# Kernel tuning notes

Measured on AMD Instinct MI355X. Metric: run time of the kernel, lower is better.

Reference implementation:

```python
import jax, jax.numpy as jnp
import numpy as np

T_STEPS = 4000          # T_ms / dt = 1000 / 0.25
N_IN, N_OUT = 64, 10
HID = [1024, 1024]
DT, TAU = 0.25, 10.0
BETA = float(np.exp(-DT / TAU))   # beta_snn
THR = 1.0                          # thr_snn
SLOPE = 1.0                        # spike_snn uses slope=1.0
W_STD = 32.0                       # W_STD_CUBA

@jax.custom_vjp
def spike(u):
    # SurrogateSpike.forward: heaviside on (mem - thr)
    return (u >= 0).astype(u.dtype)

def _spike_fwd(u):
    return spike(u), u

def _spike_bwd(u, g):
    # fast-sigmoid surrogate: slope / (1 + slope*|u|)^2
    grad = SLOPE / (1.0 + SLOPE * jnp.abs(u)) ** 2
    return (g * grad,)

spike.defvjp(_spike_fwd, _spike_bwd)

def setup_inputs() -> dict:
    key = jax.random.key(0)
    ks = jax.random.split(key, 8)
    B = 16
    # Bernoulli(0.05) input spike train, time-major [T, B, N_IN]
    input_spikes = (jax.random.uniform(ks[0], (T_STEPS, B, N_IN)) < 0.05).astype(jnp.float32)
    sizes = [N_IN] + HID + [N_OUT]
    inp = {"input_spikes": input_spikes}
    for i, (n_pre, n_post) in enumerate(zip(sizes[:-1], sizes[1:])):
        # init_weight 'normal': clamp(N(0, W_STD), min=0) / n_pre
        w = jnp.maximum(jax.random.normal(ks[i + 1], (n_pre, n_post)) * W_STD, 0.0) / n_pre
        inp[f"W{i}"] = w.astype(jnp.float32)
        inp[f"b{i}"] = jnp.zeros((n_post,), jnp.float32)
    return inp

def reference(input_spikes, W0, b0, W1, b1, W2, b2):
    # Dale's law: feedforward weights clamped >= 0 in forward
    Ws = [jnp.maximum(W, 0.0) for W in (W0, W1, W2)]
    bs = [b0, b1, b2]
    B = input_spikes.shape[1]
    sizes = HID + [N_OUT]
    mems0 = tuple(jnp.zeros((B, n), input_spikes.dtype) for n in sizes)

    def step(mems, s_in):
        s = s_in
        new_mems = []
        for l in range(len(Ws)):
            I = s @ Ws[l] + bs[l]                 # [B, n_post]
            m = BETA * mems[l] + I                # LIF decay + drive
            sp = spike(m - THR)                   # surrogate-grad spike
            m = jnp.where(sp > 0, 0.0, m)         # hard reset to zero
            new_mems.append(m)
            s = sp
        return tuple(new_mems), s                 # emit output-layer spikes

    _, out_spikes = jax.lax.scan(step, mems0, input_spikes)
    return out_spikes  # [T, B, N_OUT]
```

## Files before the change

### kernel.cpp

```cpp
#include <hip/hip_runtime.h>
#include <hip/hip_bf16.h>
#include <math.h>


#define T_STEPS 4000
#define NB 16
#define N_IN 64
#define NH 1024
#define N_OUT 10
#define SEGO 40
#define SEGH 40

typedef __attribute__((ext_vector_type(8))) short bf16x8;
typedef __attribute__((ext_vector_type(4))) float f32x4;
typedef __hip_bfloat16 bf16;
typedef unsigned long long u64;

#define ASG(p) (const __attribute__((address_space(1))) void*)(p)
#define ASL(p) (__attribute__((address_space(3))) void*)(p)


__global__ void k_zero(float* p, int n) {
    int i = blockIdx.x * 256 + threadIdx.x;
    if (i < n) p[i] = 0.f;
}

__global__ void k_mask(const float* __restrict__ in, u64* __restrict__ mask, int total) {
    int w = (blockIdx.x * 256 + threadIdx.x) >> 6;
    int lane = threadIdx.x & 63;
    if (w >= total) return;
    float v = in[(size_t)w * 64 + lane];
    u64 bal = __ballot(v > 0.5f);
    if (lane == 0) mask[w] = bal;
}

__global__ void k_unpack(const u64* __restrict__ BITS, float* __restrict__ out,
                         int total) {
    int idx = blockIdx.x * 256 + threadIdx.x;
    if (idx >= total) return;
    int t   = idx / (NB * N_OUT);
    int rem = idx - t * (NB * N_OUT);
    int b = rem / N_OUT;
    int k = rem - b * N_OUT;
    u64 w = BITS[(size_t)(t / SEGO) * 256 + b * 16 + k];
    out[idx] = ((w >> (t % SEGO)) & 1ULL) ? 1.f : 0.f;
}

__global__ __launch_bounds__(256) void k_limbs_t(
    const float* __restrict__ W, bf16* __restrict__ BT) {
    __shared__ float Wlds[64][65];
    const int tid  = threadIdx.x;
    const int lane = tid & 63;
    const int wr   = tid >> 6;
    const int k0 = (blockIdx.x & 15) * 64;
    const int n0 = (blockIdx.x >> 4) * 64;
#pragma unroll
    for (int rr = 0; rr < 16; ++rr) {
        int kl = wr * 16 + rr;
        Wlds[kl][lane] = W[(size_t)(k0 + kl) * 1024 + n0 + lane];
    }
    __syncthreads();
#pragma unroll
    for (int rr = 0; rr < 16; ++rr) {
        int nl = wr * 16 + rr;
        float w = fmaxf(Wlds[lane][nl], 0.f);
        bf16 h = __float2bfloat16(w);
        float hf = __bfloat162float(h);
        bf16 l = __float2bfloat16(w - hf);
        size_t base = (size_t)(n0 + nl) * 2048 + k0 + lane;
        BT[base] = h;
        BT[base + 1024] = l;
    }
}

__global__ void k_limbs(const float* __restrict__ W, bf16* __restrict__ BT,
                        int K, int N, int Npad) {
    int idx = blockIdx.x * 256 + threadIdx.x;
    int total = Npad * 2 * K;
    if (idx >= total) return;
    int n  = idx / (2 * K);
    int k2 = idx - n * (2 * K);
    int lo = (k2 >= K);
    int k = lo ? (k2 - K) : k2;
    float v = 0.f;
    if (n < N) {
        float w = fmaxf(W[(size_t)k * N + n], 0.f);
        float hi = __bfloat162float(__float2bfloat16(w));
        v = lo ? (w - hi) : w;
    }
    BT[idx] = __float2bfloat16(v);
}


__global__ __launch_bounds__(256) void k_gemm_thin(
    const bf16* __restrict__ A, const bf16* __restrict__ BT,
    float* __restrict__ C) {
    const int tid  = threadIdx.x;
    const int lane = tid & 63;
    const int wave = tid >> 6;
    const int r16 = lane & 15;
    const int kg  = lane >> 4;
    const int m0 = blockIdx.x * 64 + wave * 16;
    f32x4 acc = {};
    const bf16* ap = A + (size_t)(m0 + r16) * 1024 + kg * 8;
    const bf16* bh = BT + (size_t)r16 * 2048 + kg * 8;
    const bf16* bl = bh + 1024;
#pragma unroll 8
    for (int kt = 0; kt < 32; ++kt) {
        const int ka = kt * 32;
        bf16x8 af  = *(const bf16x8*)(ap + ka);
        bf16x8 bfh = *(const bf16x8*)(bh + ka);
        bf16x8 bfl = *(const bf16x8*)(bl + ka);
        acc = __builtin_amdgcn_mfma_f32_16x16x32_bf16(af, bfh, acc, 0, 0, 0);
        acc = __builtin_amdgcn_mfma_f32_16x16x32_bf16(af, bfl, acc, 0, 0, 0);
    }
#pragma unroll
    for (int rr = 0; rr < 4; ++rr)
        C[(size_t)(m0 + kg * 4 + rr) * 16 + r16] = acc[rr];
}


__global__ __launch_bounds__(512) void k_gemm8(
    const bf16* __restrict__ A, const bf16* __restrict__ BT,
    float* __restrict__ C, int gx) {
    const int KA = 1024, K2 = 2048;
    const int kmask = KA - 1;
    const int nwg = gridDim.x;
    const int wg  = blockIdx.x;
    const int q = nwg >> 3, r = nwg & 7;
    const int xcd = wg & 7, idx0 = wg >> 3;
    const int swz = (xcd < r ? xcd * (q + 1) : r * (q + 1) + (xcd - r) * q) + idx0;
    const int gy = nwg / gx;
    const int n0 = (swz % gy) * 256;
    const int m0 = (swz / gy) * 256;

    __shared__ __align__(16) char LDS[131072];
    const int tid  = threadIdx.x;
    const int lane = tid & 63;
    const int wave = tid >> 6;
    const int wm = (wave >> 2) * 128;
    const int wn = (wave & 3) * 64;
    const int r16l = lane & 15;
    const int kg   = lane >> 4;
    const int hA   = wave >> 2;
    const int hB   = (wave & 3) >> 1;
    const int wn64 = wave & 1;

    const int po = (r16l * 64 + kg * 16) ^ (((r16l >> 3) & 1) << 5);
    const char* bA[2] = { LDS + hA * 16384 + po,
                          LDS + 65536 + hA * 16384 + po };
    const char* bB[2] = { LDS + 32768 + hB * 16384 + po,
                          LDS + 98304 + hB * 16384 + po };
    const int bOff = wn64 * 8192;

    int s_row[2], s_col[2];
#pragma unroll
    for (int rr = 0; rr < 2; ++rr) {
        int d = (rr * 512 + tid) * 16;
        int l = d ^ (((d >> 9) & 1) << 5);
        int sub = l >> 10;
        int w = l & 1023;
        s_row[rr] = (sub >> 1) * 16 + (w >> 6);
        s_col[rr] = ((sub & 1) * 64 + (w & 63)) >> 1;
    }

#define HBASE(BUF, OP, HALF) ((((BUF) * 2 + (OP)) * 2 + (HALF)) * 16384)
#define STAGE_A(BUF, HALF, K0)                                              \
    {                                                                       \
        _Pragma("unroll")                                                   \
        for (int rr = 0; rr < 2; ++rr)                                      \
            __builtin_amdgcn_global_load_lds(                               \
                ASG(A + (size_t)(m0 + (HALF) * 128 + s_row[rr]) * KA        \
                    + (((K0) + s_col[rr]) & kmask)),                        \
                ASL(LDS + HBASE(BUF, 0, HALF) + (rr * 512 + wave * 64) * 16), \
                16, 0, 0);                                                  \
    }
#define STAGE_B(BUF, HALF, K0)                                              \
    {                                                                       \
        _Pragma("unroll")                                                   \
        for (int rr = 0; rr < 2; ++rr)                                      \
            __builtin_amdgcn_global_load_lds(                               \
                ASG(BT + (size_t)(n0 + (HALF) * 128 + s_row[rr]) * K2       \
                    + (K0) + s_col[rr]),                                    \
                ASL(LDS + HBASE(BUF, 1, HALF) + (rr * 512 + wave * 64) * 16), \
                16, 0, 0);                                                  \
    }

    f32x4 acc[8][4] = {};
    bf16x8 a[4][2], b[4][2];

#define MM(MIB, NIB)                                                        \
    {                                                                       \
        _Pragma("unroll")                                                   \
        for (int i = 0; i < 4; ++i)                                         \
            _Pragma("unroll")                                               \
            for (int j = 0; j < 2; ++j) {                                   \
                acc[(MIB) + i][(NIB) + j] =                                 \
                    __builtin_amdgcn_mfma_f32_16x16x32_bf16(                \
                        a[i][0], b[(NIB) + j][0], acc[(MIB) + i][(NIB) + j], 0, 0, 0); \
                acc[(MIB) + i][(NIB) + j] =                                 \
                    __builtin_amdgcn_mfma_f32_16x16x32_bf16(                \
                        a[i][1], b[(NIB) + j][1], acc[(MIB) + i][(NIB) + j], 0, 0, 0); \
            }                                                               \
    }

#define PH_SYNC()                                                           \
    __builtin_amdgcn_s_barrier();                                           \
    asm volatile("s_waitcnt lgkmcnt(0)" ::: "memory");                      \
    __builtin_amdgcn_sched_barrier(0);

#define KTILE(BUF, SK)                                                      \
    {                                                                       \
        _Pragma("unroll")                                                   \
        for (int i = 0; i < 4; ++i) {                                       \
            a[i][0] = *(const bf16x8*)(bA[BUF] + i * 2048);                 \
            a[i][1] = *(const bf16x8*)(bA[BUF] + i * 2048 + 1024);          \
        }                                                                   \
        _Pragma("unroll")                                                   \
        for (int j = 0; j < 2; ++j) {                                       \
            b[j][0] = *(const bf16x8*)(bB[BUF] + bOff + j * 2048);          \
            b[j][1] = *(const bf16x8*)(bB[BUF] + bOff + j * 2048 + 1024);   \
        }                                                                   \
        PH_SYNC();                                                          \
        __builtin_amdgcn_s_setprio(1);                                      \
        MM(0, 0);                                                           \
        __builtin_amdgcn_s_setprio(0);                                      \
        __builtin_amdgcn_s_barrier();                                       \
        _Pragma("unroll")                                                   \
        for (int j = 0; j < 2; ++j) {                                       \
            b[2 + j][0] = *(const bf16x8*)(bB[BUF] + bOff + (2 + j) * 2048); \
            b[2 + j][1] = *(const bf16x8*)(bB[BUF] + bOff + (2 + j) * 2048 + 1024); \
        }                                                                   \
        PH_SYNC();                                                          \
        __builtin_amdgcn_s_setprio(1);                                      \
        MM(0, 2);                                                           \
        __builtin_amdgcn_s_setprio(0);                                      \
        __builtin_amdgcn_s_barrier();                                       \
        _Pragma("unroll")                                                   \
        for (int i = 0; i < 4; ++i) {                                       \
            a[i][0] = *(const bf16x8*)(bA[BUF] + (4 + i) * 2048);           \
            a[i][1] = *(const bf16x8*)(bA[BUF] + (4 + i) * 2048 + 1024);    \
        }                                                                   \
        STAGE_B(BUF, 0, SK);                                                \
        STAGE_B(BUF, 1, SK);                                                \
        PH_SYNC();                                                          \
        __builtin_amdgcn_s_setprio(1);                                      \
        MM(4, 0);                                                           \
        __builtin_amdgcn_s_setprio(0);                                      \
        __builtin_amdgcn_s_barrier();                                       \
        STAGE_A(BUF, 0, SK);                                                \
        STAGE_A(BUF, 1, SK);                                                \
        PH_SYNC();                                                          \
        __builtin_amdgcn_s_setprio(1);                                      \
        MM(4, 2);                                                           \
        __builtin_amdgcn_s_setprio(0);                                      \
        asm volatile("s_waitcnt vmcnt(8)" ::: "memory");                    \
        __builtin_amdgcn_sched_barrier(0);                                  \
        __builtin_amdgcn_s_barrier();                                       \
    }

    STAGE_A(0, 0, 0);  STAGE_A(0, 1, 0);  STAGE_B(0, 0, 0);  STAGE_B(0, 1, 0);
    STAGE_A(1, 0, 64); STAGE_A(1, 1, 64); STAGE_B(1, 0, 64); STAGE_B(1, 1, 64);
    asm volatile("s_waitcnt vmcnt(8)" ::: "memory");
    __builtin_amdgcn_sched_barrier(0);
    __builtin_amdgcn_s_barrier();

    for (int it = 0; it < 16; ++it) {
        const int k0  = it * 128;
        const int ksA = (k0 + 128) & (K2 - 1);
        const int ksB = (k0 + 192) & (K2 - 1);
        KTILE(0, ksA);
        KTILE(1, ksB);
    }
    asm volatile("s_waitcnt vmcnt(0)" ::: "memory");
    __builtin_amdgcn_sched_barrier(0);

#pragma unroll
    for (int mi = 0; mi < 8; ++mi)
#pragma unroll
        for (int ni = 0; ni < 4; ++ni)
#pragma unroll
            for (int rr = 0; rr < 4; ++rr) {
                int row = m0 + wm + mi * 16 + kg * 4 + rr;
                int col = n0 + wn + ni * 16 + r16l;
                C[(size_t)row * 1024 + col] = acc[mi][ni][rr];
            }
#undef KTILE
#undef PH_SYNC
#undef MM
#undef STAGE_A
#undef STAGE_B
#undef HBASE
}


__global__ __launch_bounds__(64) void k_scan_l0(
    const u64* __restrict__ mask,
    const float* __restrict__ W0,
    const float* __restrict__ bias,
    float* __restrict__ mstate, bf16* __restrict__ S, int Tc, float beta) {
    __shared__ float Ilds[2][16][68];
    const int lane = threadIdx.x;
    const int gid  = blockIdx.x * 64 + lane;
    const int b  = blockIdx.x >> 4;
    const int q  = blockIdx.x & 15;
    const int j0 = q * 64;
    const int r16 = lane & 15;
    const int kg  = lane >> 4;
    bf16x8 bh[4][2], bl[4][2];
#pragma unroll
    for (int jt = 0; jt < 4; ++jt)
#pragma unroll
        for (int kk = 0; kk < 2; ++kk)
#pragma unroll
            for (int e = 0; e < 8; ++e) {
                int k = kk * 32 + kg * 8 + e;
                float w = fmaxf(W0[(size_t)k * 1024 + j0 + jt * 16 + r16], 0.f);
                bf16 h = __float2bfloat16(w);
                float hf = __bfloat162float(h);
                bf16 l = __float2bfloat16(w - hf);
                bh[jt][kk][e] = *(short*)&h;
                bl[jt][kk][e] = *(short*)&l;
            }
    float m = mstate[gid];
    const float bj = bias[j0 + lane];
    const size_t stride = (size_t)NB * NH;
    const int ntile = Tc / 16;
    const int tmax = ntile - 1;

#define LOADM(TT) mask[(size_t)(((TT) <= tmax ? (TT) : tmax) * 16 + r16) * NB + b]

#define L0_COMPUTE(MSK, P)                                                  \
    {                                                                       \
        f32x4 acc[4] = {};                                                  \
        _Pragma("unroll")                                                   \
        for (int kk = 0; kk < 2; ++kk) {                                    \
            unsigned byte8 = (unsigned)(((MSK) >> (kk * 32 + kg * 8)) & 0xFF); \
            bf16x8 af;                                                      \
            _Pragma("unroll")                                               \
            for (int e = 0; e < 8; ++e)                                     \
                af[e] = ((byte8 >> e) & 1) ? (short)0x3F80 : (short)0;      \
            _Pragma("unroll")                                               \
            for (int jt = 0; jt < 4; ++jt) {                                \
                acc[jt] = __builtin_amdgcn_mfma_f32_16x16x32_bf16(          \
                    af, bh[jt][kk], acc[jt], 0, 0, 0);                      \
                acc[jt] = __builtin_amdgcn_mfma_f32_16x16x32_bf16(          \
                    af, bl[jt][kk], acc[jt], 0, 0, 0);                      \
            }                                                               \
        }                                                                   \
        _Pragma("unroll")                                                   \
        for (int jt = 0; jt < 4; ++jt)                                      \
            _Pragma("unroll")                                               \
            for (int rr = 0; rr < 4; ++rr)                                  \
                Ilds[P][kg * 4 + rr][jt * 16 + r16] = acc[jt][rr];          \
    }

    u64 mc = LOADM(0);
    L0_COMPUTE(mc, 0);
    u64 mn = LOADM(1);
    for (int tt = 0; tt < ntile; ++tt) {
        __builtin_amdgcn_s_barrier();
        float v[16];
#pragma unroll
        for (int u = 0; u < 16; ++u)
            v[u] = Ilds[tt & 1][u][lane];
        u64 m2 = LOADM(tt + 2);
        if (tt + 1 < ntile) L0_COMPUTE(mn, (tt + 1) & 1);
        unsigned short o[16];
#pragma unroll
        for (int u = 0; u < 16; ++u) {
            m = fmaf(beta, m, v[u] + bj);
            bool sp = (m >= 1.0f);
            o[u] = sp ? (unsigned short)0x3F80 : (unsigned short)0;
            m = sp ? 0.f : m;
        }
#pragma unroll
        for (int u = 0; u < 16; ++u)
            ((unsigned short*)S)[(size_t)(tt * 16 + u) * stride + gid] = o[u];
        mn = m2;
    }
    mstate[gid] = m;
#undef L0_COMPUTE
#undef LOADM
}

__global__ __launch_bounds__(64) void k_scan_hidden(
    const float* __restrict__ I, const float* __restrict__ bias,
    float* __restrict__ mstate, bf16* __restrict__ S, int Tc, float beta) {
    __shared__ __align__(16) float segA[SEGH * 64];
    __shared__ __align__(16) float segB[SEGH * 64];
    const int lane = threadIdx.x;
    const int gid  = blockIdx.x * 64 + lane;
    const int j = gid & (NH - 1);
    float m = mstate[gid];
    const float bj = bias[j];
    const size_t stride = (size_t)NB * NH;
    const int nseg = Tc / SEGH;
    const int lrow = lane >> 4;
    const int lcol = (lane & 15) << 2;

#define H_PREFETCH(SEGBUF, SIDX)                                            \
    {                                                                       \
        const float* src = I + (size_t)(SIDX) * SEGH * stride               \
                             + (size_t)lrow * stride + blockIdx.x * 64 + lcol; \
        _Pragma("unroll")                                                   \
        for (int g = 0; g < SEGH / 4; ++g)                                  \
            __builtin_amdgcn_global_load_lds(                               \
                ASG(src + (size_t)(g * 4) * stride),                        \
                ASL(&SEGBUF[g * 256]), 16, 0, 0);                           \
    }

#define H_PROC(SEGBUF, SIDX)                                                \
    {                                                                       \
        const int btt = (SIDX) * SEGH;                                      \
        _Pragma("unroll")                                                   \
        for (int sb = 0; sb < SEGH / 8; ++sb) {                             \
            float v[8];                                                     \
            _Pragma("unroll")                                               \
            for (int u = 0; u < 8; ++u)                                     \
                v[u] = SEGBUF[(sb * 8 + u) * 64 + lane];                    \
            unsigned short o[8];                                            \
            _Pragma("unroll")                                               \
            for (int u = 0; u < 8; ++u) {                                   \
                m = fmaf(beta, m, v[u] + bj);                               \
                bool sp = (m >= 1.0f);                                      \
                o[u] = sp ? (unsigned short)0x3F80 : (unsigned short)0;     \
                m = sp ? 0.f : m;                                           \
            }                                                               \
            _Pragma("unroll")                                               \
            for (int u = 0; u < 8; ++u)                                     \
                ((unsigned short*)S)[(size_t)(btt + sb * 8 + u) * stride + gid] = o[u]; \
        }                                                                   \
    }

    H_PREFETCH(segA, 0);
    H_PREFETCH(segB, 1);
    asm volatile("s_waitcnt vmcnt(10)" ::: "memory");
    __builtin_amdgcn_sched_barrier(0);
    for (int s = 0; s < nseg; s += 2) {
        H_PROC(segA, s);
        if (s + 2 < nseg) {
            H_PREFETCH(segA, s + 2);
            asm volatile("s_waitcnt vmcnt(50)" ::: "memory");
        } else {
            asm volatile("s_waitcnt vmcnt(40)" ::: "memory");
        }
        __builtin_amdgcn_sched_barrier(0);
        H_PROC(segB, s + 1);
        if (s + 3 < nseg) {
            H_PREFETCH(segB, s + 3);
            asm volatile("s_waitcnt vmcnt(50)" ::: "memory");
            __builtin_amdgcn_sched_barrier(0);
        } else if (s + 2 < nseg) {
            asm volatile("s_waitcnt vmcnt(40)" ::: "memory");
            __builtin_amdgcn_sched_barrier(0);
        }
    }
    mstate[gid] = m;
#undef H_PREFETCH
#undef H_PROC
}

__global__ __launch_bounds__(256) void k_scan_out(
    const float* __restrict__ I2, const float* __restrict__ bias,
    float* __restrict__ mstate, u64* __restrict__ BITS,
    int Tc, float beta) {
    __shared__ __align__(16) float segA[SEGO * 256];
    __shared__ __align__(16) float segB[SEGO * 256];
    const int tid  = threadIdx.x;
    const int lane = tid & 63;
    const int wave = tid >> 6;
    const int k = tid & 15;
    float m = mstate[tid];
    float bj = (k < N_OUT) ? bias[k] : 0.f;
    const int nseg = Tc / SEGO;

#define O_PREFETCH(SEGBUF, SIDX)                                            \
    {                                                                       \
        const float* src = I2 + (size_t)(SIDX) * SEGO * 256                 \
                              + (size_t)wave * 256 + lane * 4;              \
        _Pragma("unroll")                                                   \
        for (int g = 0; g < SEGO / 4; ++g)                                  \
            __builtin_amdgcn_global_load_lds(                               \
                ASG(src + (size_t)(g * 4) * 256),                           \
                ASL(&SEGBUF[(g * 4 + wave) * 256]), 16, 0, 0);              \
    }

#define O_PROC(SEGBUF, SIDX)                                                \
    {                                                                       \
        u64 obits = 0;                                                      \
        _Pragma("unroll")                                                   \
        for (int sb = 0; sb < SEGO / 8; ++sb) {                             \
            float v[8];                                                     \
            _Pragma("unroll")                                               \
            for (int u = 0; u < 8; ++u)                                     \
                v[u] = SEGBUF[(sb * 8 + u) * 256 + tid];                    \
            _Pragma("unroll")                                               \
            for (int u = 0; u < 8; ++u) {                                   \
                m = fmaf(beta, m, v[u] + bj);                               \
                bool sp = (m >= 1.0f);                                      \
                obits |= ((u64)(sp ? 1 : 0)) << (sb * 8 + u);               \
                m = sp ? 0.f : m;                                           \
            }                                                               \
        }                                                                   \
        BITS[(size_t)(SIDX) * 256 + tid] = obits;                           \
    }

    O_PREFETCH(segA, 0);
    O_PREFETCH(segB, 1);
    asm volatile("s_waitcnt vmcnt(10)" ::: "memory");
    __builtin_amdgcn_sched_barrier(0);
    __builtin_amdgcn_s_barrier();
    for (int s = 0; s < nseg; s += 2) {
        O_PROC(segA, s);
        if (s + 2 < nseg) {
            O_PREFETCH(segA, s + 2);
            asm volatile("s_waitcnt vmcnt(11)" ::: "memory");
        } else {
            asm volatile("s_waitcnt vmcnt(1)" ::: "memory");
        }
        __builtin_amdgcn_sched_barrier(0);
        __builtin_amdgcn_s_barrier();
        O_PROC(segB, s + 1);
        if (s + 3 < nseg) {
            O_PREFETCH(segB, s + 3);
            asm volatile("s_waitcnt vmcnt(11)" ::: "memory");
            __builtin_amdgcn_sched_barrier(0);
            __builtin_amdgcn_s_barrier();
        } else if (s + 2 < nseg) {
            asm volatile("s_waitcnt vmcnt(1)" ::: "memory");
            __builtin_amdgcn_sched_barrier(0);
            __builtin_amdgcn_s_barrier();
        }
    }
    mstate[tid] = m;
#undef O_PREFETCH
#undef O_PROC
}


extern "C" void kernel_launch(void* const* d_in, const int* in_sizes, int n_in,
                              void* d_out, int out_size, void* d_ws, size_t ws_size,
                              hipStream_t stream) {
    const float* in_sp = (const float*)d_in[0];
    const float* W0 = (const float*)d_in[1];
    const float* b0 = (const float*)d_in[2];
    const float* W1 = (const float*)d_in[3];
    const float* b1 = (const float*)d_in[4];
    const float* W2 = (const float*)d_in[5];
    const float* b2 = (const float*)d_in[6];
    float* out = (float*)d_out;

    char* p = (char*)d_ws;
    auto carve = [&](size_t bytes) -> void* {
        char* r = p; p += (bytes + 255) & ~(size_t)255; return (void*)r;
    };
    u64*  MASK  = (u64*)carve((size_t)T_STEPS * NB * 8);
    bf16* BT1   = (bf16*)carve((size_t)NH * 2 * NH * 2);
    bf16* BT2   = (bf16*)carve((size_t)128 * 2 * NH * 2);
    float* m0s  = (float*)carve((size_t)NB * NH * 4);
    float* m1s  = (float*)carve((size_t)NB * NH * 4);
    float* m2s  = (float*)carve((size_t)NB * 16 * 4);
    float* I2BUF = (float*)carve((size_t)T_STEPS * NB * 16 * 4);
    u64*  BITS  = (u64*)carve((size_t)(T_STEPS / SEGO) * 256 * 8);
    size_t fixed = (size_t)(p - (char*)d_ws);

    const int tc_opts[3] = {2000, 800, 400};
    int Tc = 400;
    for (int i = 0; i < 3; ++i) {
        size_t Mc_ = (size_t)tc_opts[i] * NB;
        size_t need = fixed
            + ((Mc_ * NH * 4 + 255) & ~(size_t)255)
            + ((Mc_ * NH * 2 + 255) & ~(size_t)255);
        if (need <= ws_size) { Tc = tc_opts[i]; break; }
    }
    size_t Mc = (size_t)Tc * NB;
    float* IBUF = (float*)carve(Mc * NH * 4);
    bf16*  S    = (bf16*)carve(Mc * NH * 2);

    const float beta = (float)exp(-0.25 / 10.0);

    int nM = NB * NH * 2 + NB * 16;
    k_zero<<<(nM + 255) / 256, 256, 0, stream>>>(m0s, nM);

    k_mask<<<(T_STEPS * NB * 64) / 256, 256, 0, stream>>>(in_sp, MASK, T_STEPS * NB);

    k_limbs_t<<<256, 256, 0, stream>>>(W1, BT1);
    k_limbs<<<(128 * 2 * NH + 255) / 256, 256, 0, stream>>>(W2, BT2, NH, N_OUT, 128);

    const int C = T_STEPS / Tc;
    const int gx8 = (int)(Mc / 256);
    const int gthin = (int)(Mc / 64);
    for (int c = 0; c < C; ++c) {
        int t0 = c * Tc;
        k_scan_l0<<<256, 64, 0, stream>>>(MASK + (size_t)t0 * NB, W0, b0,
                                          m0s, S, Tc, beta);
        k_gemm8<<<gx8 * 4, 512, 0, stream>>>(S, BT1, IBUF, gx8);
        k_scan_hidden<<<(NB * NH) / 64, 64, 0, stream>>>(IBUF, b1, m1s, S, Tc, beta);
        k_gemm_thin<<<gthin, 256, 0, stream>>>(S, BT2,
                                               I2BUF + (size_t)t0 * NB * 16);
    }
    k_scan_out<<<1, 256, 0, stream>>>(I2BUF, b2, m2s, BITS, T_STEPS, beta);
    int nOut = T_STEPS * NB * N_OUT;
    k_unpack<<<(nOut + 255) / 256, 256, 0, stream>>>(BITS, out, nOut);
}
```

Before: 729.2 us.

## Store hidden spikes as packed bitmasks and expand via LDS lookup in GEMMs

The scan kernels now pack each 64-neuron spike vector into a u64 with a wave ballot instead of writing one bf16 per neuron. Both GEMM kernels load these bitmasks and expand each byte into a bf16x8 A-fragment through a 256-entry lookup table in LDS. This cuts the spike-matrix traffic sixteenfold and frees LDS in the large GEMM. The cost is extra LDS lookups and scalar bit extraction inside the MFMA loop, plus one store per lane-0 per timestep in the scans.

```diff
diff --git a/kernel.cpp b/kernel.cpp
--- a/kernel.cpp
+++ b/kernel.cpp
@@ -93,26 +93,40 @@
 
 
 __global__ __launch_bounds__(256) void k_gemm_thin(
-    const bf16* __restrict__ A, const bf16* __restrict__ BT,
+    const u64* __restrict__ SB, const bf16* __restrict__ BT,
     float* __restrict__ C) {
+    __shared__ __align__(16) short LUT[256 * 8];
     const int tid  = threadIdx.x;
+    if (tid < 256) {
+        bf16x8 e;
+#pragma unroll
+        for (int i = 0; i < 8; ++i)
+            e[i] = ((tid >> i) & 1) ? (short)0x3F80 : (short)0;
+        *(bf16x8*)&LUT[tid * 8] = e;
+    }
+    __syncthreads();
     const int lane = tid & 63;
     const int wave = tid >> 6;
     const int r16 = lane & 15;
     const int kg  = lane >> 4;
     const int m0 = blockIdx.x * 64 + wave * 16;
     f32x4 acc = {};
-    const bf16* ap = A + (size_t)(m0 + r16) * 1024 + kg * 8;
+    const u64* mp = SB + (size_t)(m0 + r16) * 16;
     const bf16* bh = BT + (size_t)r16 * 2048 + kg * 8;
     const bf16* bl = bh + 1024;
-#pragma unroll 8
-    for (int kt = 0; kt < 32; ++kt) {
-        const int ka = kt * 32;
-        bf16x8 af  = *(const bf16x8*)(ap + ka);
-        bf16x8 bfh = *(const bf16x8*)(bh + ka);
-        bf16x8 bfl = *(const bf16x8*)(bl + ka);
-        acc = __builtin_amdgcn_mfma_f32_16x16x32_bf16(af, bfh, acc, 0, 0, 0);
-        acc = __builtin_amdgcn_mfma_f32_16x16x32_bf16(af, bfl, acc, 0, 0, 0);
+#pragma unroll 4
+    for (int w = 0; w < 16; ++w) {
+        u64 mk = mp[w];
+#pragma unroll
+        for (int half = 0; half < 2; ++half) {
+            int ka = w * 64 + half * 32;
+            unsigned by = (unsigned)(mk >> (half * 32 + kg * 8)) & 0xFF;
+            bf16x8 af  = *(const bf16x8*)&LUT[by * 8];
+            bf16x8 bfh = *(const bf16x8*)(bh + ka);
+            bf16x8 bfl = *(const bf16x8*)(bl + ka);
+            acc = __builtin_amdgcn_mfma_f32_16x16x32_bf16(af, bfh, acc, 0, 0, 0);
+            acc = __builtin_amdgcn_mfma_f32_16x16x32_bf16(af, bfl, acc, 0, 0, 0);
+        }
     }
 #pragma unroll
     for (int rr = 0; rr < 4; ++rr)
@@ -121,10 +135,9 @@
 
 
 __global__ __launch_bounds__(512) void k_gemm8(
-    const bf16* __restrict__ A, const bf16* __restrict__ BT,
+    const u64* __restrict__ SB, const bf16* __restrict__ BT,
     float* __restrict__ C, int gx) {
-    const int KA = 1024, K2 = 2048;
-    const int kmask = KA - 1;
+    const int K2 = 2048;
     const int nwg = gridDim.x;
     const int wg  = blockIdx.x;
     const int q = nwg >> 3, r = nwg & 7;
@@ -134,7 +147,7 @@
     const int n0 = (swz % gy) * 256;
     const int m0 = (swz / gy) * 256;
 
-    __shared__ __align__(16) char LDS[131072];
+    __shared__ __align__(16) char LDS[73728];
     const int tid  = threadIdx.x;
     const int lane = tid & 63;
     const int wave = tid >> 6;
@@ -142,15 +155,22 @@
     const int wn = (wave & 3) * 64;
     const int r16l = lane & 15;
     const int kg   = lane >> 4;
-    const int hA   = wave >> 2;
     const int hB   = (wave & 3) >> 1;
     const int wn64 = wave & 1;
 
+    if (tid < 256) {
+        bf16x8 e;
+#pragma unroll
+        for (int i = 0; i < 8; ++i)
+            e[i] = ((tid >> i) & 1) ? (short)0x3F80 : (short)0;
+        *(bf16x8*)(LDS + tid * 16) = e;
+    }
+    __syncthreads();
+
+    const char* AMb[2] = { LDS + 4096, LDS + 6144 };
     const int po = (r16l * 64 + kg * 16) ^ (((r16l >> 3) & 1) << 5);
-    const char* bA[2] = { LDS + hA * 16384 + po,
-                          LDS + 65536 + hA * 16384 + po };
-    const char* bB[2] = { LDS + 32768 + hB * 16384 + po,
-                          LDS + 98304 + hB * 16384 + po };
+    const char* bB[2] = { LDS + 8192 + hB * 16384 + po,
+                          LDS + 8192 + 32768 + hB * 16384 + po };
     const int bOff = wn64 * 8192;
 
     int s_row[2], s_col[2];
@@ -164,17 +184,6 @@
         s_col[rr] = ((sub & 1) * 64 + (w & 63)) >> 1;
     }
 
-#define HBASE(BUF, OP, HALF) ((((BUF) * 2 + (OP)) * 2 + (HALF)) * 16384)
-#define STAGE_A(BUF, HALF, K0)                                              \
-    {                                                                       \
-        _Pragma("unroll")                                                   \
-        for (int rr = 0; rr < 2; ++rr)                                      \
-            __builtin_amdgcn_global_load_lds(                               \
-                ASG(A + (size_t)(m0 + (HALF) * 128 + s_row[rr]) * KA        \
-                    + (((K0) + s_col[rr]) & kmask)),                        \
-                ASL(LDS + HBASE(BUF, 0, HALF) + (rr * 512 + wave * 64) * 16), \
-                16, 0, 0);                                                  \
-    }
 #define STAGE_B(BUF, HALF, K0)                                              \
     {                                                                       \
         _Pragma("unroll")                                                   \
@@ -182,12 +191,30 @@
             __builtin_amdgcn_global_load_lds(                               \
                 ASG(BT + (size_t)(n0 + (HALF) * 128 + s_row[rr]) * K2       \
                     + (K0) + s_col[rr]),                                    \
-                ASL(LDS + HBASE(BUF, 1, HALF) + (rr * 512 + wave * 64) * 16), \
+                ASL(LDS + 8192 + (BUF) * 32768 + (HALF) * 16384             \
+                    + (rr * 512 + wave * 64) * 16),                         \
                 16, 0, 0);                                                  \
     }
+#define STAGE_AM(BUF, WORD)                                                 \
+    __builtin_amdgcn_global_load_lds(                                       \
+        ASG((const char*)SB + (size_t)(m0 + (tid >> 1)) * 128               \
+            + (WORD) * 8 + (tid & 1) * 4),                                  \
+        ASL(LDS + 4096 + (BUF) * 2048 + tid * 4), 4, 0, 0);
 
     f32x4 acc[8][4] = {};
     bf16x8 a[4][2], b[4][2];
+
+#define AFRAG(BUF, IB)                                                      \
+    {                                                                       \
+        _Pragma("unroll")                                                   \
+        for (int i = 0; i < 4; ++i) {                                       \
+            u64 mk = *(const u64*)(AMb[BUF] + (wm + ((IB) + i) * 16 + r16l) * 8); \
+            unsigned b0_ = (unsigned)(mk >> (kg * 8)) & 0xFF;               \
+            unsigned b1_ = (unsigned)((mk >> 32) >> (kg * 8)) & 0xFF;       \
+            a[i][0] = *(const bf16x8*)(LDS + b0_ * 16);                     \
+            a[i][1] = *(const bf16x8*)(LDS + b1_ * 16);                     \
+        }                                                                   \
+    }
 
 #define MM(MIB, NIB)                                                        \
     {                                                                       \
@@ -211,11 +238,8 @@
 
 #define KTILE(BUF, SK)                                                      \
     {                                                                       \
-        _Pragma("unroll")                                                   \
-        for (int i = 0; i < 4; ++i) {                                       \
-            a[i][0] = *(const bf16x8*)(bA[BUF] + i * 2048);                 \
-            a[i][1] = *(const bf16x8*)(bA[BUF] + i * 2048 + 1024);          \
-        }                                                                   \
+                                   \
+        AFRAG(BUF, 0);                                                      \
         _Pragma("unroll")                                                   \
         for (int j = 0; j < 2; ++j) {                                       \
             b[j][0] = *(const bf16x8*)(bB[BUF] + bOff + j * 2048);          \
@@ -226,6 +250,7 @@
         MM(0, 0);                                                           \
         __builtin_amdgcn_s_setprio(0);                                      \
         __builtin_amdgcn_s_barrier();                                       \
+                                                            \
         _Pragma("unroll")                                                   \
         for (int j = 0; j < 2; ++j) {                                       \
             b[2 + j][0] = *(const bf16x8*)(bB[BUF] + bOff + (2 + j) * 2048); \
@@ -236,11 +261,8 @@
         MM(0, 2);                                                           \
         __builtin_amdgcn_s_setprio(0);                                      \
         __builtin_amdgcn_s_barrier();                                       \
-        _Pragma("unroll")                                                   \
-        for (int i = 0; i < 4; ++i) {                                       \
-            a[i][0] = *(const bf16x8*)(bA[BUF] + (4 + i) * 2048);           \
-            a[i][1] = *(const bf16x8*)(bA[BUF] + (4 + i) * 2048 + 1024);    \
-        }                                                                   \
+                        \
+        AFRAG(BUF, 4);                                                      \
         STAGE_B(BUF, 0, SK);                                                \
         STAGE_B(BUF, 1, SK);                                                \
         PH_SYNC();                                                          \
@@ -248,20 +270,20 @@
         MM(4, 0);                                                           \
         __builtin_amdgcn_s_setprio(0);                                      \
         __builtin_amdgcn_s_barrier();                                       \
-        STAGE_A(BUF, 0, SK);                                                \
-        STAGE_A(BUF, 1, SK);                                                \
+                      \
+        STAGE_AM(BUF, ((SK) >> 6) & 15);                                    \
         PH_SYNC();                                                          \
         __builtin_amdgcn_s_setprio(1);                                      \
         MM(4, 2);                                                           \
         __builtin_amdgcn_s_setprio(0);                                      \
-        asm volatile("s_waitcnt vmcnt(8)" ::: "memory");                    \
+        asm volatile("s_waitcnt vmcnt(5)" ::: "memory");                    \
         __builtin_amdgcn_sched_barrier(0);                                  \
         __builtin_amdgcn_s_barrier();                                       \
     }
 
-    STAGE_A(0, 0, 0);  STAGE_A(0, 1, 0);  STAGE_B(0, 0, 0);  STAGE_B(0, 1, 0);
-    STAGE_A(1, 0, 64); STAGE_A(1, 1, 64); STAGE_B(1, 0, 64); STAGE_B(1, 1, 64);
-    asm volatile("s_waitcnt vmcnt(8)" ::: "memory");
+    STAGE_AM(0, 0); STAGE_B(0, 0, 0);  STAGE_B(0, 1, 0);
+    STAGE_AM(1, 1); STAGE_B(1, 0, 64); STAGE_B(1, 1, 64);
+    asm volatile("s_waitcnt vmcnt(5)" ::: "memory");
     __builtin_amdgcn_sched_barrier(0);
     __builtin_amdgcn_s_barrier();
 
@@ -288,9 +310,9 @@
 #undef KTILE
 #undef PH_SYNC
 #undef MM
-#undef STAGE_A
+#undef AFRAG
+#undef STAGE_AM
 #undef STAGE_B
-#undef HBASE
 }
 
 
@@ -298,7 +320,7 @@
     const u64* __restrict__ mask,
     const float* __restrict__ W0,
     const float* __restrict__ bias,
-    float* __restrict__ mstate, bf16* __restrict__ S, int Tc, float beta) {
+    float* __restrict__ mstate, u64* __restrict__ SBITS, int Tc, float beta) {
     __shared__ float Ilds[2][16][68];
     const int lane = threadIdx.x;
     const int gid  = blockIdx.x * 64 + lane;
@@ -324,7 +346,6 @@
             }
     float m = mstate[gid];
     const float bj = bias[j0 + lane];
-    const size_t stride = (size_t)NB * NH;
     const int ntile = Tc / 16;
     const int tmax = ntile - 1;
 
@@ -366,17 +387,15 @@
             v[u] = Ilds[tt & 1][u][lane];
         u64 m2 = LOADM(tt + 2);
         if (tt + 1 < ntile) L0_COMPUTE(mn, (tt + 1) & 1);
-        unsigned short o[16];
 #pragma unroll
         for (int u = 0; u < 16; ++u) {
             m = fmaf(beta, m, v[u] + bj);
             bool sp = (m >= 1.0f);
-            o[u] = sp ? (unsigned short)0x3F80 : (unsigned short)0;
+            u64 bal = __ballot(sp);
+            if (lane == 0)
+                SBITS[((size_t)(tt * 16 + u) * 16 + b) * 16 + q] = bal;
             m = sp ? 0.f : m;
         }
-#pragma unroll
-        for (int u = 0; u < 16; ++u)
-            ((unsigned short*)S)[(size_t)(tt * 16 + u) * stride + gid] = o[u];
         mn = m2;
     }
     mstate[gid] = m;
@@ -386,11 +405,13 @@
 
 __global__ __launch_bounds__(64) void k_scan_hidden(
     const float* __restrict__ I, const float* __restrict__ bias,
-    float* __restrict__ mstate, bf16* __restrict__ S, int Tc, float beta) {
+    float* __restrict__ mstate, u64* __restrict__ SBITS, int Tc, float beta) {
     __shared__ __align__(16) float segA[SEGH * 64];
     __shared__ __align__(16) float segB[SEGH * 64];
     const int lane = threadIdx.x;
     const int gid  = blockIdx.x * 64 + lane;
+    const int b = blockIdx.x >> 4;
+    const int q = blockIdx.x & 15;
     const int j = gid & (NH - 1);
     float m = mstate[gid];
     const float bj = bias[j];
@@ -419,17 +440,15 @@
             _Pragma("unroll")                                               \
             for (int u = 0; u < 8; ++u)                                     \
                 v[u] = SEGBUF[(sb * 8 + u) * 64 + lane];                    \
-            unsigned short o[8];                                            \
             _Pragma("unroll")                                               \
             for (int u = 0; u < 8; ++u) {                                   \
                 m = fmaf(beta, m, v[u] + bj);                               \
                 bool sp = (m >= 1.0f);                                      \
-                o[u] = sp ? (unsigned short)0x3F80 : (unsigned short)0;     \
+                u64 bal = __ballot(sp);                                     \
+                if (lane == 0)                                              \
+                    SBITS[((size_t)(btt + sb * 8 + u) * 16 + b) * 16 + q] = bal; \
                 m = sp ? 0.f : m;                                           \
             }                                                               \
-            _Pragma("unroll")                                               \
-            for (int u = 0; u < 8; ++u)                                     \
-                ((unsigned short*)S)[(size_t)(btt + sb * 8 + u) * stride + gid] = o[u]; \
         }                                                                   \
     }
 
@@ -571,12 +590,12 @@
         size_t Mc_ = (size_t)tc_opts[i] * NB;
         size_t need = fixed
             + ((Mc_ * NH * 4 + 255) & ~(size_t)255)
-            + ((Mc_ * NH * 2 + 255) & ~(size_t)255);
+            + ((Mc_ * 16 * 8 + 255) & ~(size_t)255);
         if (need <= ws_size) { Tc = tc_opts[i]; break; }
     }
     size_t Mc = (size_t)Tc * NB;
-    float* IBUF = (float*)carve(Mc * NH * 4);
-    bf16*  S    = (bf16*)carve(Mc * NH * 2);
+    float* IBUF  = (float*)carve(Mc * NH * 4);
+    u64*   SBITS = (u64*)carve(Mc * 16 * 8);
 
     const float beta = (float)exp(-0.25 / 10.0);
 
@@ -594,10 +613,10 @@
     for (int c = 0; c < C; ++c) {
         int t0 = c * Tc;
         k_scan_l0<<<256, 64, 0, stream>>>(MASK + (size_t)t0 * NB, W0, b0,
-                                          m0s, S, Tc, beta);
-        k_gemm8<<<gx8 * 4, 512, 0, stream>>>(S, BT1, IBUF, gx8);
-        k_scan_hidden<<<(NB * NH) / 64, 64, 0, stream>>>(IBUF, b1, m1s, S, Tc, beta);
-        k_gemm_thin<<<gthin, 256, 0, stream>>>(S, BT2,
+                                          m0s, SBITS, Tc, beta);
+        k_gemm8<<<gx8 * 4, 512, 0, stream>>>(SBITS, BT1, IBUF, gx8);
+        k_scan_hidden<<<(NB * NH) / 64, 64, 0, stream>>>(IBUF, b1, m1s, SBITS, Tc, beta);
+        k_gemm_thin<<<gthin, 256, 0, stream>>>(SBITS, BT2,
                                                I2BUF + (size_t)t0 * NB * 16);
     }
     k_scan_out<<<1, 256, 0, stream>>>(I2BUF, b2, m2s, BITS, T_STEPS, beta);
```

After: 902.3 us. 1.24x slower.

## Pack hidden-layer spikes as ballot bitmasks and expand via LDS LUT in thin GEMM

Applied to the files above, without the earlier changes.

The hidden-layer scan now writes each timestep's spikes as one 64-bit ballot mask per 64 neurons instead of a bf16 value per neuron. The thin output GEMM reads these masks and expands each byte into a bf16x8 operand through a 256-entry LDS lookup table. This is meant to cut the spike traffic between the two kernels by about 16x. In exchange it adds a per-block LUT build with a barrier, serial per-step lane-0 stores in the scan, and an extra workspace buffer that may force a smaller Tc.

```diff
diff --git a/kernel.cpp b/kernel.cpp
--- a/kernel.cpp
+++ b/kernel.cpp
@@ -93,26 +93,40 @@
 
 
 __global__ __launch_bounds__(256) void k_gemm_thin(
-    const bf16* __restrict__ A, const bf16* __restrict__ BT,
+    const u64* __restrict__ SB, const bf16* __restrict__ BT,
     float* __restrict__ C) {
+    __shared__ __align__(16) short LUT[256 * 8];
     const int tid  = threadIdx.x;
+    if (tid < 256) {
+        bf16x8 e;
+#pragma unroll
+        for (int i = 0; i < 8; ++i)
+            e[i] = ((tid >> i) & 1) ? (short)0x3F80 : (short)0;
+        *(bf16x8*)&LUT[tid * 8] = e;
+    }
+    __syncthreads();
     const int lane = tid & 63;
     const int wave = tid >> 6;
     const int r16 = lane & 15;
     const int kg  = lane >> 4;
     const int m0 = blockIdx.x * 64 + wave * 16;
     f32x4 acc = {};
-    const bf16* ap = A + (size_t)(m0 + r16) * 1024 + kg * 8;
+    const u64* mp = SB + (size_t)(m0 + r16) * 16;
     const bf16* bh = BT + (size_t)r16 * 2048 + kg * 8;
     const bf16* bl = bh + 1024;
-#pragma unroll 8
-    for (int kt = 0; kt < 32; ++kt) {
-        const int ka = kt * 32;
-        bf16x8 af  = *(const bf16x8*)(ap + ka);
-        bf16x8 bfh = *(const bf16x8*)(bh + ka);
-        bf16x8 bfl = *(const bf16x8*)(bl + ka);
-        acc = __builtin_amdgcn_mfma_f32_16x16x32_bf16(af, bfh, acc, 0, 0, 0);
-        acc = __builtin_amdgcn_mfma_f32_16x16x32_bf16(af, bfl, acc, 0, 0, 0);
+#pragma unroll 4
+    for (int w = 0; w < 16; ++w) {
+        u64 mk = mp[w];
+#pragma unroll
+        for (int half = 0; half < 2; ++half) {
+            int ka = w * 64 + half * 32;
+            unsigned by = (unsigned)(mk >> (half * 32 + kg * 8)) & 0xFF;
+            bf16x8 af  = *(const bf16x8*)&LUT[by * 8];
+            bf16x8 bfh = *(const bf16x8*)(bh + ka);
+            bf16x8 bfl = *(const bf16x8*)(bl + ka);
+            acc = __builtin_amdgcn_mfma_f32_16x16x32_bf16(af, bfh, acc, 0, 0, 0);
+            acc = __builtin_amdgcn_mfma_f32_16x16x32_bf16(af, bfl, acc, 0, 0, 0);
+        }
     }
 #pragma unroll
     for (int rr = 0; rr < 4; ++rr)
@@ -386,11 +400,13 @@
 
 __global__ __launch_bounds__(64) void k_scan_hidden(
     const float* __restrict__ I, const float* __restrict__ bias,
-    float* __restrict__ mstate, bf16* __restrict__ S, int Tc, float beta) {
+    float* __restrict__ mstate, u64* __restrict__ SBITS, int Tc, float beta) {
     __shared__ __align__(16) float segA[SEGH * 64];
     __shared__ __align__(16) float segB[SEGH * 64];
     const int lane = threadIdx.x;
     const int gid  = blockIdx.x * 64 + lane;
+    const int b = blockIdx.x >> 4;
+    const int q = blockIdx.x & 15;
     const int j = gid & (NH - 1);
     float m = mstate[gid];
     const float bj = bias[j];
@@ -419,17 +435,15 @@
             _Pragma("unroll")                                               \
             for (int u = 0; u < 8; ++u)                                     \
                 v[u] = SEGBUF[(sb * 8 + u) * 64 + lane];                    \
-            unsigned short o[8];                                            \
             _Pragma("unroll")                                               \
             for (int u = 0; u < 8; ++u) {                                   \
                 m = fmaf(beta, m, v[u] + bj);                               \
                 bool sp = (m >= 1.0f);                                      \
-                o[u] = sp ? (unsigned short)0x3F80 : (unsigned short)0;     \
+                u64 bal = __ballot(sp);                                     \
+                if (lane == 0)                                              \
+                    SBITS[((size_t)(btt + sb * 8 + u) * 16 + b) * 16 + q] = bal; \
                 m = sp ? 0.f : m;                                           \
             }                                                               \
-            _Pragma("unroll")                                               \
-            for (int u = 0; u < 8; ++u)                                     \
-                ((unsigned short*)S)[(size_t)(btt + sb * 8 + u) * stride + gid] = o[u]; \
         }                                                                   \
     }
 
@@ -571,12 +585,14 @@
         size_t Mc_ = (size_t)tc_opts[i] * NB;
         size_t need = fixed
             + ((Mc_ * NH * 4 + 255) & ~(size_t)255)
-            + ((Mc_ * NH * 2 + 255) & ~(size_t)255);
+            + ((Mc_ * NH * 2 + 255) & ~(size_t)255)
+            + ((Mc_ * 16 * 8 + 255) & ~(size_t)255);
         if (need <= ws_size) { Tc = tc_opts[i]; break; }
     }
     size_t Mc = (size_t)Tc * NB;
-    float* IBUF = (float*)carve(Mc * NH * 4);
-    bf16*  S    = (bf16*)carve(Mc * NH * 2);
+    float* IBUF  = (float*)carve(Mc * NH * 4);
+    bf16*  S     = (bf16*)carve(Mc * NH * 2);
+    u64*   SBITS = (u64*)carve(Mc * 16 * 8);
 
     const float beta = (float)exp(-0.25 / 10.0);
 
@@ -596,8 +612,8 @@
         k_scan_l0<<<256, 64, 0, stream>>>(MASK + (size_t)t0 * NB, W0, b0,
                                           m0s, S, Tc, beta);
         k_gemm8<<<gx8 * 4, 512, 0, stream>>>(S, BT1, IBUF, gx8);
-        k_scan_hidden<<<(NB * NH) / 64, 64, 0, stream>>>(IBUF, b1, m1s, S, Tc, beta);
-        k_gemm_thin<<<gthin, 256, 0, stream>>>(S, BT2,
+        k_scan_hidden<<<(NB * NH) / 64, 64, 0, stream>>>(IBUF, b1, m1s, SBITS, Tc, beta);
+        k_gemm_thin<<<gthin, 256, 0, stream>>>(SBITS, BT2,
                                                I2BUF + (size_t)t0 * NB * 16);
     }
     k_scan_out<<<1, 256, 0, stream>>>(I2BUF, b2, m2s, BITS, T_STEPS, beta);
```

Result: slower. 769.6 us (+5.5%).

## Overlap output-layer scan with next chunk's GEMM and fuse prep kernels

Applied to the files above, without the earlier changes.

Merges the four setup kernels (zeroing, input bit-masking, W1 and W2 limb conversion) into one launch that branches on block index. The single-block output-layer scan no longer runs once serially over all 4000 steps at the end. Each chunk's output scan now runs inside an extra block of the next chunk's GEMM launch, and only the last chunk is scanned afterwards. This hides most of the serial scan behind GEMM work, at the cost of one GEMM block's slot and the tail block's dependence on the previous chunk's thin-GEMM output.

```diff
diff --git a/kernel.cpp b/kernel.cpp
--- a/kernel.cpp
+++ b/kernel.cpp
@@ -20,18 +20,70 @@
 #define ASL(p) (__attribute__((address_space(3))) void*)(p)
 
 
-__global__ void k_zero(float* p, int n) {
-    int i = blockIdx.x * 256 + threadIdx.x;
-    if (i < n) p[i] = 0.f;
-}
-
-__global__ void k_mask(const float* __restrict__ in, u64* __restrict__ mask, int total) {
-    int w = (blockIdx.x * 256 + threadIdx.x) >> 6;
-    int lane = threadIdx.x & 63;
-    if (w >= total) return;
-    float v = in[(size_t)w * 64 + lane];
-    u64 bal = __ballot(v > 0.5f);
-    if (lane == 0) mask[w] = bal;
+__global__ __launch_bounds__(256) void k_prep(
+    const float* __restrict__ in_sp, u64* __restrict__ mask,
+    const float* __restrict__ W1, bf16* __restrict__ BT1,
+    const float* __restrict__ W2, bf16* __restrict__ BT2,
+    float* __restrict__ mst, int nM, int ZB, int MB) {
+    __shared__ float Wlds[64][65];
+    int b = blockIdx.x;
+    const int tid = threadIdx.x;
+    if (b < ZB) {
+        int i = b * 256 + tid;
+        if (i < nM) mst[i] = 0.f;
+        return;
+    }
+    b -= ZB;
+    if (b < MB) {
+        int w = b * 4 + (tid >> 6);
+        int lane = tid & 63;
+        float v = in_sp[(size_t)w * 64 + lane];
+        u64 bal = __ballot(v > 0.5f);
+        if (lane == 0) mask[w] = bal;
+        return;
+    }
+    b -= MB;
+    if (b < 256) {
+        const int lane = tid & 63;
+        const int wr   = tid >> 6;
+        const int k0 = (b & 15) * 64;
+        const int n0 = (b >> 4) * 64;
+#pragma unroll
+        for (int rr = 0; rr < 16; ++rr) {
+            int kl = wr * 16 + rr;
+            Wlds[kl][lane] = W1[(size_t)(k0 + kl) * 1024 + n0 + lane];
+        }
+        __syncthreads();
+#pragma unroll
+        for (int rr = 0; rr < 16; ++rr) {
+            int nl = wr * 16 + rr;
+            float w = fmaxf(Wlds[lane][nl], 0.f);
+            bf16 h = __float2bfloat16(w);
+            float hf = __bfloat162float(h);
+            bf16 l = __float2bfloat16(w - hf);
+            size_t base = (size_t)(n0 + nl) * 2048 + k0 + lane;
+            BT1[base] = h;
+            BT1[base + 1024] = l;
+        }
+        return;
+    }
+    b -= 256;
+    {
+        int idx = b * 256 + tid;
+        int total = 128 * 2 * NH;
+        if (idx >= total) return;
+        int n  = idx / (2 * NH);
+        int k2 = idx - n * (2 * NH);
+        int lo = (k2 >= NH);
+        int k = lo ? (k2 - NH) : k2;
+        float v = 0.f;
+        if (n < N_OUT) {
+            float w = fmaxf(W2[(size_t)k * N_OUT + n], 0.f);
+            float hi = __bfloat162float(__float2bfloat16(w));
+            v = lo ? (w - hi) : w;
+        }
+        BT2[idx] = __float2bfloat16(v);
+    }
 }
 
 __global__ void k_unpack(const u64* __restrict__ BITS, float* __restrict__ out,
@@ -46,49 +98,93 @@
     out[idx] = ((w >> (t % SEGO)) & 1ULL) ? 1.f : 0.f;
 }
 
-__global__ __launch_bounds__(256) void k_limbs_t(
-    const float* __restrict__ W, bf16* __restrict__ BT) {
-    __shared__ float Wlds[64][65];
-    const int tid  = threadIdx.x;
+
+__device__ __forceinline__ void scan_out_body(
+    const float* __restrict__ I2, const float* __restrict__ bias,
+    float* __restrict__ mstate, u64* __restrict__ BITS,
+    int Tc, float* seg, int tid) {
+    float* segA = seg;
+    float* segB = seg + SEGO * 256;
+    const bool act = tid < 256;
     const int lane = tid & 63;
-    const int wr   = tid >> 6;
-    const int k0 = (blockIdx.x & 15) * 64;
-    const int n0 = (blockIdx.x >> 4) * 64;
-#pragma unroll
-    for (int rr = 0; rr < 16; ++rr) {
-        int kl = wr * 16 + rr;
-        Wlds[kl][lane] = W[(size_t)(k0 + kl) * 1024 + n0 + lane];
-    }
-    __syncthreads();
-#pragma unroll
-    for (int rr = 0; rr < 16; ++rr) {
-        int nl = wr * 16 + rr;
-        float w = fmaxf(Wlds[lane][nl], 0.f);
-        bf16 h = __float2bfloat16(w);
-        float hf = __bfloat162float(h);
-        bf16 l = __float2bfloat16(w - hf);
-        size_t base = (size_t)(n0 + nl) * 2048 + k0 + lane;
-        BT[base] = h;
-        BT[base + 1024] = l;
-    }
-}
-
-__global__ void k_limbs(const float* __restrict__ W, bf16* __restrict__ BT,
-                        int K, int N, int Npad) {
-    int idx = blockIdx.x * 256 + threadIdx.x;
-    int total = Npad * 2 * K;
-    if (idx >= total) return;
-    int n  = idx / (2 * K);
-    int k2 = idx - n * (2 * K);
-    int lo = (k2 >= K);
-    int k = lo ? (k2 - K) : k2;
-    float v = 0.f;
-    if (n < N) {
-        float w = fmaxf(W[(size_t)k * N + n], 0.f);
-        float hi = __bfloat162float(__float2bfloat16(w));
-        v = lo ? (w - hi) : w;
-    }
-    BT[idx] = __float2bfloat16(v);
+    const int wave = tid >> 6;
+    const int k = tid & 15;
+    float m = 0.f, bj = 0.f;
+    if (act) {
+        m = mstate[tid];
+        bj = (k < N_OUT) ? bias[k] : 0.f;
+    }
+    const int nseg = Tc / SEGO;
+
+#define O_PREFETCH(SEGBUF, SIDX)                                            \
+    if (act) {                                                              \
+        const float* src = I2 + (size_t)(SIDX) * SEGO * 256                 \
+                              + (size_t)wave * 256 + lane * 4;              \
+        _Pragma("unroll")                                                   \
+        for (int g = 0; g < SEGO / 4; ++g)                                  \
+            __builtin_amdgcn_global_load_lds(                               \
+                ASG(src + (size_t)(g * 4) * 256),                           \
+                ASL(&SEGBUF[(g * 4 + wave) * 256]), 16, 0, 0);              \
+    }
+
+#define O_PROC(SEGBUF, SIDX)                                                \
+    if (act) {                                                              \
+        u64 obits = 0;                                                      \
+        _Pragma("unroll")                                                   \
+        for (int sb = 0; sb < SEGO / 8; ++sb) {                             \
+            float v[8];                                                     \
+            _Pragma("unroll")                                               \
+            for (int u = 0; u < 8; ++u)                                     \
+                v[u] = SEGBUF[(sb * 8 + u) * 256 + tid];                    \
+            _Pragma("unroll")                                               \
+            for (int u = 0; u < 8; ++u) {                                   \
+                m = fmaf(beta_c, m, v[u] + bj);                             \
+                bool sp = (m >= 1.0f);                                      \
+                obits |= ((u64)(sp ? 1 : 0)) << (sb * 8 + u);               \
+                m = sp ? 0.f : m;                                           \
+            }                                                               \
+        }                                                                   \
+        BITS[(size_t)(SIDX) * 256 + tid] = obits;                           \
+    }
+
+    const float beta_c = 0.97530991202833261687f;
+    O_PREFETCH(segA, 0);
+    O_PREFETCH(segB, 1);
+    asm volatile("s_waitcnt vmcnt(10)" ::: "memory");
+    __builtin_amdgcn_sched_barrier(0);
+    __builtin_amdgcn_s_barrier();
+    for (int s = 0; s < nseg; s += 2) {
+        O_PROC(segA, s);
+        if (s + 2 < nseg) {
+            O_PREFETCH(segA, s + 2);
+            asm volatile("s_waitcnt vmcnt(11)" ::: "memory");
+        } else {
+            asm volatile("s_waitcnt vmcnt(1)" ::: "memory");
+        }
+        __builtin_amdgcn_sched_barrier(0);
+        __builtin_amdgcn_s_barrier();
+        O_PROC(segB, s + 1);
+        if (s + 3 < nseg) {
+            O_PREFETCH(segB, s + 3);
+            asm volatile("s_waitcnt vmcnt(11)" ::: "memory");
+            __builtin_amdgcn_sched_barrier(0);
+            __builtin_amdgcn_s_barrier();
+        } else if (s + 2 < nseg) {
+            asm volatile("s_waitcnt vmcnt(1)" ::: "memory");
+            __builtin_amdgcn_sched_barrier(0);
+            __builtin_amdgcn_s_barrier();
+        }
+    }
+    if (act) mstate[tid] = m;
+#undef O_PREFETCH
+#undef O_PROC
+}
+
+__global__ __launch_bounds__(256) void k_scan_out(
+    const float* __restrict__ I2, const float* __restrict__ bias,
+    float* __restrict__ mstate, u64* __restrict__ BITS, int Tc) {
+    __shared__ __align__(16) float seg[2 * SEGO * 256];
+    scan_out_body(I2, bias, mstate, BITS, Tc, seg, threadIdx.x);
 }
 
 
@@ -122,10 +218,20 @@
 
 __global__ __launch_bounds__(512) void k_gemm8(
     const bf16* __restrict__ A, const bf16* __restrict__ BT,
-    float* __restrict__ C, int gx) {
+    float* __restrict__ C, int gx,
+    const float* __restrict__ I2t, const float* __restrict__ b2t,
+    float* __restrict__ m2t, u64* __restrict__ BITSt, int tcT, int doTail) {
+    __shared__ __align__(16) char LDS[131072];
+    const int tid  = threadIdx.x;
+
+    if (doTail && (int)blockIdx.x == (int)gridDim.x - 1) {
+        scan_out_body(I2t, b2t, m2t, BITSt, tcT, (float*)LDS, tid);
+        return;
+    }
+
     const int KA = 1024, K2 = 2048;
     const int kmask = KA - 1;
-    const int nwg = gridDim.x;
+    const int nwg = gridDim.x - doTail;
     const int wg  = blockIdx.x;
     const int q = nwg >> 3, r = nwg & 7;
     const int xcd = wg & 7, idx0 = wg >> 3;
@@ -134,8 +240,6 @@
     const int n0 = (swz % gy) * 256;
     const int m0 = (swz / gy) * 256;
 
-    __shared__ __align__(16) char LDS[131072];
-    const int tid  = threadIdx.x;
     const int lane = tid & 63;
     const int wave = tid >> 6;
     const int wm = (wave >> 2) * 128;
@@ -461,83 +565,6 @@
 #undef H_PROC
 }
 
-__global__ __launch_bounds__(256) void k_scan_out(
-    const float* __restrict__ I2, const float* __restrict__ bias,
-    float* __restrict__ mstate, u64* __restrict__ BITS,
-    int Tc, float beta) {
-    __shared__ __align__(16) float segA[SEGO * 256];
-    __shared__ __align__(16) float segB[SEGO * 256];
-    const int tid  = threadIdx.x;
-    const int lane = tid & 63;
-    const int wave = tid >> 6;
-    const int k = tid & 15;
-    float m = mstate[tid];
-    float bj = (k < N_OUT) ? bias[k] : 0.f;
-    const int nseg = Tc / SEGO;
-
-#define O_PREFETCH(SEGBUF, SIDX)                                            \
-    {                                                                       \
-        const float* src = I2 + (size_t)(SIDX) * SEGO * 256                 \
-                              + (size_t)wave * 256 + lane * 4;              \
-        _Pragma("unroll")                                                   \
-        for (int g = 0; g < SEGO / 4; ++g)                                  \
-            __builtin_amdgcn_global_load_lds(                               \
-                ASG(src + (size_t)(g * 4) * 256),                           \
-                ASL(&SEGBUF[(g * 4 + wave) * 256]), 16, 0, 0);              \
-    }
-
-#define O_PROC(SEGBUF, SIDX)                                                \
-    {                                                                       \
-        u64 obits = 0;                                                      \
-        _Pragma("unroll")                                                   \
-        for (int sb = 0; sb < SEGO / 8; ++sb) {                             \
-            float v[8];                                                     \
-            _Pragma("unroll")                                               \
-            for (int u = 0; u < 8; ++u)                                     \
-                v[u] = SEGBUF[(sb * 8 + u) * 256 + tid];                    \
-            _Pragma("unroll")                                               \
-            for (int u = 0; u < 8; ++u) {                                   \
-                m = fmaf(beta, m, v[u] + bj);                               \
-                bool sp = (m >= 1.0f);                                      \
-                obits |= ((u64)(sp ? 1 : 0)) << (sb * 8 + u);               \
-                m = sp ? 0.f : m;                                           \
-            }                                                               \
-        }                                                                   \
-        BITS[(size_t)(SIDX) * 256 + tid] = obits;                           \
-    }
-
-    O_PREFETCH(segA, 0);
-    O_PREFETCH(segB, 1);
-    asm volatile("s_waitcnt vmcnt(10)" ::: "memory");
-    __builtin_amdgcn_sched_barrier(0);
-    __builtin_amdgcn_s_barrier();
-    for (int s = 0; s < nseg; s += 2) {
-        O_PROC(segA, s);
-        if (s + 2 < nseg) {
-            O_PREFETCH(segA, s + 2);
-            asm volatile("s_waitcnt vmcnt(11)" ::: "memory");
-        } else {
-            asm volatile("s_waitcnt vmcnt(1)" ::: "memory");
-        }
-        __builtin_amdgcn_sched_barrier(0);
-        __builtin_amdgcn_s_barrier();
-        O_PROC(segB, s + 1);
-        if (s + 3 < nseg) {
-            O_PREFETCH(segB, s + 3);
-            asm volatile("s_waitcnt vmcnt(11)" ::: "memory");
-            __builtin_amdgcn_sched_barrier(0);
-            __builtin_amdgcn_s_barrier();
-        } else if (s + 2 < nseg) {
-            asm volatile("s_waitcnt vmcnt(1)" ::: "memory");
-            __builtin_amdgcn_sched_barrier(0);
-            __builtin_amdgcn_s_barrier();
-        }
-    }
-    mstate[tid] = m;
-#undef O_PREFETCH
-#undef O_PROC
-}
-
 
 extern "C" void kernel_launch(void* const* d_in, const int* in_sizes, int n_in,
                               void* d_out, int out_size, void* d_ws, size_t ws_size,
@@ -581,12 +608,11 @@
     const float beta = (float)exp(-0.25 / 10.0);
 
     int nM = NB * NH * 2 + NB * 16;
-    k_zero<<<(nM + 255) / 256, 256, 0, stream>>>(m0s, nM);
-
-    k_mask<<<(T_STEPS * NB * 64) / 256, 256, 0, stream>>>(in_sp, MASK, T_STEPS * NB);
-
-    k_limbs_t<<<256, 256, 0, stream>>>(W1, BT1);
-    k_limbs<<<(128 * 2 * NH + 255) / 256, 256, 0, stream>>>(W2, BT2, NH, N_OUT, 128);
+    const int ZB = (nM + 255) / 256;
+    const int MB = (T_STEPS * NB) / 4;
+    const int L2B = (128 * 2 * NH + 255) / 256;
+    k_prep<<<ZB + MB + 256 + L2B, 256, 0, stream>>>(
+        in_sp, MASK, W1, BT1, W2, BT2, m0s, nM, ZB, MB);
 
     const int C = T_STEPS / Tc;
     const int gx8 = (int)(Mc / 256);
@@ -595,12 +621,24 @@
         int t0 = c * Tc;
         k_scan_l0<<<256, 64, 0, stream>>>(MASK + (size_t)t0 * NB, W0, b0,
                                           m0s, S, Tc, beta);
-        k_gemm8<<<gx8 * 4, 512, 0, stream>>>(S, BT1, IBUF, gx8);
+        if (c == 0) {
+            k_gemm8<<<gx8 * 4, 512, 0, stream>>>(S, BT1, IBUF, gx8,
+                                                 nullptr, nullptr, nullptr,
+                                                 nullptr, 0, 0);
+        } else {
+            int tp = (c - 1) * Tc;
+            k_gemm8<<<gx8 * 4 + 1, 512, 0, stream>>>(
+                S, BT1, IBUF, gx8,
+                I2BUF + (size_t)tp * NB * 16, b2, m2s,
+                BITS + (size_t)(tp / SEGO) * 256, Tc, 1);
+        }
         k_scan_hidden<<<(NB * NH) / 64, 64, 0, stream>>>(IBUF, b1, m1s, S, Tc, beta);
         k_gemm_thin<<<gthin, 256, 0, stream>>>(S, BT2,
                                                I2BUF + (size_t)t0 * NB * 16);
     }
-    k_scan_out<<<1, 256, 0, stream>>>(I2BUF, b2, m2s, BITS, T_STEPS, beta);
+    int tl = (C - 1) * Tc;
+    k_scan_out<<<1, 256, 0, stream>>>(I2BUF + (size_t)tl * NB * 16, b2, m2s,
+                                      BITS + (size_t)(tl / SEGO) * 256, Tc);
     int nOut = T_STEPS * NB * N_OUT;
     k_unpack<<<(nOut + 255) / 256, 256, 0, stream>>>(BITS, out, nOut);
 }
```

Result: faster. 672.1 us (-7.8%).
